# Performance work log

Measured on AMD Instinct MI355X. Metric: run time of the kernel, lower is better.

The kernel has to match this reference:

```python
import jax, jax.numpy as jnp
import numpy as np

EPS = 1e-5
H, D = 8, 64  # n_heads, head_n_channels


def _instance_norm(x):
    # x: [B, H, N, D]; InstanceNorm1d over grid axis N per (batch, head, channel)
    m = jnp.mean(x, axis=2, keepdims=True)
    v = jnp.var(x, axis=2, keepdims=True)
    return (x - m) * jax.lax.rsqrt(v + EPS)


def setup_inputs() -> dict:
    key = jax.random.key(0)
    ks = jax.random.split(key, 7)
    B, N, C, OUT = 4, 16384, 256, 256
    u_src = jax.random.normal(ks[0], (B, N, C), jnp.float32)
    pos_src = jax.random.uniform(ks[1], (B, N, 2), jnp.float32)
    s_in = 1.0 / np.sqrt(C)
    Wq = jax.random.normal(ks[2], (H * D, C), jnp.float32) * s_in
    Wk = jax.random.normal(ks[3], (H * D, C), jnp.float32) * s_in
    Wv = jax.random.normal(ks[4], (H * D, C), jnp.float32) * s_in
    Wo = jax.random.normal(ks[5], (OUT, H * D), jnp.float32) * (1.0 / np.sqrt(H * D))
    bo = jnp.zeros((OUT,), jnp.float32)
    return {"u_src": u_src, "pos_src": pos_src, "Wq": Wq, "Wk": Wk, "Wv": Wv, "Wo": Wo, "bo": bo}


def reference(u_src, pos_src, Wq, Wk, Wv, Wo, bo):
    B, N, C = u_src.shape
    # q/k/v projections -> [B, H, N, D]
    q = (u_src @ Wq.T).reshape(B, N, H, D).transpose(0, 2, 1, 3)
    k = (u_src @ Wk.T).reshape(B, N, H, D).transpose(0, 2, 1, 3)
    v = (u_src @ Wv.T).reshape(B, N, H, D).transpose(0, 2, 1, 3)
    # instance-norm k, v over the grid (domain) axis
    k = _instance_norm(k)
    v = _instance_norm(v)
    # associative linear attention with uniform quadrature weights 1/N
    w = 1.0 / N
    kv = jnp.einsum('bhnd,bhne->bhde', k, v * w)   # [B,H,D,D]
    u = jnp.einsum('bhnd,bhde->bhne', q, kv)       # [B,H,N,D]
    u = u.transpose(0, 2, 1, 3).reshape(B, N, H * D)
    return u @ Wo.T + bo
```

## Files before the change

kernel.cpp:

```cpp
#include <hip/hip_runtime.h>
#include <hip/hip_bf16.h>

#define BB    4
#define NTOT  16384
#define CC    256
#define HH    8
#define DD    64
#define HD    512
#define OUTC  256

typedef unsigned short u16;
typedef unsigned int u32;
typedef __attribute__((ext_vector_type(8))) short bf16x8;
typedef __attribute__((ext_vector_type(4))) float f32x4;
typedef __attribute__((ext_vector_type(4))) short u16x4;
typedef __attribute__((ext_vector_type(4))) u32 u32x4;

__device__ __forceinline__ float b2f(u16 u) {
    union { float f; u32 i; } x; x.i = ((u32)u) << 16; return x.f;
}
__device__ __forceinline__ u16 f2b(float f) {
    union { float f; u32 i; } x; x.f = f;
    u32 r = x.i + 0x7fffu + ((x.i >> 16) & 1u);
    return (u16)(r >> 16);
}

#define GLD(gp, lp) __builtin_amdgcn_global_load_lds( \
    (const __attribute__((address_space(1))) void*)(gp), \
    (__attribute__((address_space(3))) void*)(lp), 16, 0, 0)

#define MFMA(a, b, c) __builtin_amdgcn_mfma_f32_16x16x32_bf16((a), (b), (c), 0, 0, 0)

__global__ __launch_bounds__(256) void wcvt(
    const float* __restrict__ Wq, const float* __restrict__ Wk,
    const float* __restrict__ Wv, const float* __restrict__ Wo,
    u16* __restrict__ q, u16* __restrict__ k,
    u16* __restrict__ v, u16* __restrict__ o)
{
    const int z = blockIdx.z;
    const float* src = z == 0 ? Wq : z == 1 ? Wk : z == 2 ? Wv : Wo;
    u16* dst = z == 0 ? q : z == 1 ? k : z == 2 ? v : o;
    const int i = (blockIdx.x * 256 + threadIdx.x) * 8;
    const float4 a = *(const float4*)(src + i);
    const float4 b = *(const float4*)(src + i + 4);
    union { bf16x8 v; u16 s[8]; } w;
    w.s[0] = f2b(a.x); w.s[1] = f2b(a.y); w.s[2] = f2b(a.z); w.s[3] = f2b(a.w);
    w.s[4] = f2b(b.x); w.s[5] = f2b(b.y); w.s[6] = f2b(b.z); w.s[7] = f2b(b.w);
    *(bf16x8*)(dst + i) = w.v;
}

__global__ __launch_bounds__(512) void ggemm(
    const float* __restrict__ u, float* __restrict__ Gp, float* __restrict__ suP,
    u16* __restrict__ u_b)
{
    __shared__ u32 Ts[16 * 290];
    const int z = blockIdx.x, b = z >> 6, ck = z & 63;
    const float* base = u + (long long)b * NTOT * CC + (long long)ck * 256 * CC;
    u16* ub_base = u_b + (long long)b * NTOT * CC + (long long)ck * 256 * CC;
    const int t = threadIdx.x, w = t >> 6, l = t & 63;
    const int wy = w >> 1, wx = w & 1;
    const int r16 = l & 15, quad = l >> 4;
    const int sp = t >> 5;
    const int sq = t & 31;

    const int csa0 = 9 * ((wy * 64 + r16) >> 3) + (r16 & 7);
    const int csb0 = 9 * ((wx * 128 + r16) >> 3) + (r16 & 7);
    const int pr0 = 4 * quad * 290;

    f32x4 acc[4][8] = {};
    float su8[8] = {};

    float4 a0, a1, b0, b1;
    {
        const float* src = base + (long long)(2 * sp) * CC + sq * 8;
        a0 = *(const float4*)src;       a1 = *(const float4*)(src + 4);
        b0 = *(const float4*)(src + CC); b1 = *(const float4*)(src + CC + 4);
    }

    for (int it = 0; it < 8; it++) {
        {
            union { bf16x8 v; u16 q[8]; } ra, rb;
            ra.q[0] = f2b(a0.x); ra.q[1] = f2b(a0.y); ra.q[2] = f2b(a0.z); ra.q[3] = f2b(a0.w);
            ra.q[4] = f2b(a1.x); ra.q[5] = f2b(a1.y); ra.q[6] = f2b(a1.z); ra.q[7] = f2b(a1.w);
            rb.q[0] = f2b(b0.x); rb.q[1] = f2b(b0.y); rb.q[2] = f2b(b0.z); rb.q[3] = f2b(b0.w);
            rb.q[4] = f2b(b1.x); rb.q[5] = f2b(b1.y); rb.q[6] = f2b(b1.z); rb.q[7] = f2b(b1.w);
#pragma unroll
            for (int k = 0; k < 8; k++)
                su8[k] += b2f(ra.q[k]) + b2f(rb.q[k]);
            {
                u16* ub = ub_base + (long long)(it * 32 + 2 * sp) * CC + sq * 8;
                *(bf16x8*)ub = ra.v;
                *(bf16x8*)(ub + CC) = rb.v;
            }
            u32 pk[8];
#pragma unroll
            for (int k = 0; k < 8; k++)
                pk[k] = (u32)ra.q[k] | ((u32)rb.q[k] << 16);
            u32* dst = Ts + sp * 290 + 9 * sq;
#pragma unroll
            for (int k = 0; k < 8; k++) dst[k] = pk[k];
        }
        if (it < 7) {
            const float* src = base + (long long)((it + 1) * 32 + 2 * sp) * CC + sq * 8;
            a0 = *(const float4*)src;       a1 = *(const float4*)(src + 4);
            b0 = *(const float4*)(src + CC); b1 = *(const float4*)(src + CC + 4);
        }
        asm volatile("s_waitcnt lgkmcnt(0)" ::: "memory");
        __builtin_amdgcn_s_barrier();

        bf16x8 a[4], bb[8];
#pragma unroll
        for (int i = 0; i < 4; i++) {
            const int cs = csa0 + 18 * i;
            union { u32x4 u4; bf16x8 h; } f;
            f.u4[0] = Ts[pr0 + cs];       f.u4[1] = Ts[pr0 + 290 + cs];
            f.u4[2] = Ts[pr0 + 580 + cs]; f.u4[3] = Ts[pr0 + 870 + cs];
            a[i] = f.h;
        }
#pragma unroll
        for (int j = 0; j < 8; j++) {
            const int cs = csb0 + 18 * j;
            union { u32x4 u4; bf16x8 h; } f;
            f.u4[0] = Ts[pr0 + cs];       f.u4[1] = Ts[pr0 + 290 + cs];
            f.u4[2] = Ts[pr0 + 580 + cs]; f.u4[3] = Ts[pr0 + 870 + cs];
            bb[j] = f.h;
        }
#pragma unroll
        for (int i = 0; i < 4; i++)
#pragma unroll
            for (int j = 0; j < 8; j++)
                acc[i][j] = MFMA(a[i], bb[j], acc[i][j]);
        asm volatile("" ::: "memory");
        __builtin_amdgcn_s_barrier();
    }

    float* Cp = Gp + (long long)z * 65536;
#pragma unroll
    for (int i = 0; i < 4; i++)
#pragma unroll
        for (int j = 0; j < 8; j++)
#pragma unroll
            for (int rr = 0; rr < 4; rr++)
                Cp[(wy * 64 + 16 * i + quad * 4 + rr) * 256 + wx * 128 + 16 * j + r16]
                    = acc[i][j][rr];

    float* S = (float*)Ts;
#pragma unroll
    for (int k = 0; k < 8; k++) S[sp * 264 + sq * 8 + k] = su8[k];
    __syncthreads();
    if (t < 256) {
        float s = 0.f;
#pragma unroll
        for (int p = 0; p < 16; p++) s += S[p * 264 + t];
        suP[z * 256 + t] = s;
    }
}

__global__ __launch_bounds__(256) void gred(
    const float* __restrict__ Gp, const float* __restrict__ suP,
    u16* __restrict__ Gb, float* __restrict__ su)
{
    const int b = blockIdx.y, t = threadIdx.x;
    const int row = blockIdx.x * 4 + (t >> 6);
    const int col = (t & 63) * 4;
    const float* p = Gp + (long long)(b * 64) * 65536 + row * 256 + col;
    f32x4 s = {};
#pragma unroll
    for (int ck = 0; ck < 64; ck++) {
        f32x4 v = *(const f32x4*)(p + (long long)ck * 65536);
        s[0] += v[0]; s[1] += v[1]; s[2] += v[2]; s[3] += v[3];
    }
    union { u16x4 v; u16 q[4]; } pk;
#pragma unroll
    for (int k = 0; k < 4; k++) pk.q[k] = f2b(s[k]);
    *(u16x4*)(Gb + (long long)b * 65536 + row * 256 + col) = pk.v;

    if (blockIdx.x == 0) {
        float s2 = 0.f;
#pragma unroll
        for (int ck = 0; ck < 64; ck++) s2 += suP[(b * 64 + ck) * 256 + t];
        su[b * 256 + t] = s2;
    }
}

__global__ __launch_bounds__(256) void skvz(
    const u16* __restrict__ P2, const float* __restrict__ su,
    const u16* __restrict__ Wk_b, const u16* __restrict__ Wv_b,
    const u16* __restrict__ Wq_b, u16* __restrict__ Zt)
{
    __shared__ u16 pool[20480];
    __shared__ float mkL[64], rkL[64], mvL[64], rvL[64];

    const int bx = blockIdx.x, b = bx >> 3, h = bx & 7;
    const int t = threadIdx.x, w = t >> 6, l = t & 63;
    const int r16 = l & 15, quad = l >> 4;

    const u16* WkH = Wk_b + (h * 64) * 256;
    const u16* WvH = Wv_b + (h * 64) * 256;
    const u16* PkH = P2 + (long long)b * 262144 + (h * 64) * 256;
    const u16* PvH = P2 + (long long)b * 262144 + (512 + h * 64) * 256;

    {
        const int row = t >> 1, half = t & 1;
        const u16* Prow = (row < 64 ? PkH + row * 256 : PvH + (row - 64) * 256) + half * 128;
        const u16* Wrow = (row < 64 ? WkH + row * 256 : WvH + (row - 64) * 256) + half * 128;
        const float* suB = su + b * 256 + half * 128;
        float e2 = 0.f, m = 0.f;
#pragma unroll
        for (int c8 = 0; c8 < 16; c8++) {
            bf16x8 pw = *(const bf16x8*)(Prow + c8 * 8);
            bf16x8 ww = *(const bf16x8*)(Wrow + c8 * 8);
#pragma unroll
            for (int k = 0; k < 8; k++) {
                const float wv_ = b2f((u16)ww[k]);
                e2 += b2f((u16)pw[k]) * wv_;
                m  += wv_ * suB[c8 * 8 + k];
            }
        }
        e2 += __shfl_xor(e2, 1);
        m  += __shfl_xor(m, 1);
        if (half == 0) {
            m *= (1.0f / NTOT);
            const float r = rsqrtf(e2 * (1.0f / NTOT) - m * m + 1e-5f);
            if (row < 64) { mkL[row] = m; rkL[row] = r; }
            else          { mvL[row - 64] = m; rvL[row - 64] = r; }
        }
    }
    __syncthreads();

    const int mh = (w >> 1) * 32, nh = (w & 1) * 32;
    float mkR[2][4], rkR[2][4], mvR[2], rvR[2];
#pragma unroll
    for (int i = 0; i < 2; i++)
#pragma unroll
        for (int rr = 0; rr < 4; rr++) {
            mkR[i][rr] = mkL[mh + 16 * i + quad * 4 + rr];
            rkR[i][rr] = rkL[mh + 16 * i + quad * 4 + rr];
        }
#pragma unroll
    for (int j = 0; j < 2; j++) {
        mvR[j] = mvL[nh + 16 * j + r16];
        rvR[j] = rvL[nh + 16 * j + r16];
    }

    f32x4 accs[2][2] = {};
    for (int ch = 0; ch < 8; ch++) {
        const int ko = quad * 8;
        bf16x8 ap[2], bv[2];
#pragma unroll
        for (int i = 0; i < 2; i++)
            ap[i] = *(const bf16x8*)(PkH + (mh + 16 * i + r16) * 256 + ch * 32 + ko);
#pragma unroll
        for (int j = 0; j < 2; j++)
            bv[j] = *(const bf16x8*)(WvH + (nh + 16 * j + r16) * 256 + ch * 32 + ko);
#pragma unroll
        for (int i = 0; i < 2; i++)
#pragma unroll
            for (int j = 0; j < 2; j++)
                accs[i][j] = MFMA(ap[i], bv[j], accs[i][j]);
    }

    u16* kvTL = pool;
    u16* WqTL = pool + 4096;
#pragma unroll
    for (int i = 0; i < 2; i++)
#pragma unroll
        for (int j = 0; j < 2; j++)
#pragma unroll
            for (int rr = 0; rr < 4; rr++) {
                const int d = mh + 16 * i + quad * 4 + rr;
                const int e = nh + 16 * j + r16;
                const float kv = rkR[i][rr] * rvR[j] *
                    (accs[i][j][rr] * (1.0f / NTOT) - mkR[i][rr] * mvR[j]);
                kvTL[(d >> 5) * 2048 + e * 32 + (d & 31)] = f2b(kv);
            }
    {
        const int d = t >> 2, q = t & 3;
        const u16* Wrow = Wq_b + (h * 64 + d) * 256 + q * 64;
#pragma unroll
        for (int s = 0; s < 8; s++) {
            bf16x8 raw = *(const bf16x8*)(Wrow + s * 8);
#pragma unroll
            for (int k = 0; k < 8; k++) {
                const int c = q * 64 + s * 8 + k;
                WqTL[(d >> 5) * 8192 + c * 32 + (d & 31)] = (u16)raw[k];
            }
        }
    }
    __syncthreads();

    f32x4 accy[4][4] = {};
#pragma unroll
    for (int ch = 0; ch < 2; ch++) {
        const int ko = quad * 8;
        bf16x8 akv[4], bq[4];
#pragma unroll
        for (int i = 0; i < 4; i++)
            akv[i] = *(const bf16x8*)(kvTL + ch * 2048 + (16 * i + r16) * 32 + ko);
#pragma unroll
        for (int j = 0; j < 4; j++)
            bq[j] = *(const bf16x8*)(WqTL + ch * 8192 + (w * 64 + 16 * j + r16) * 32 + ko);
#pragma unroll
        for (int i = 0; i < 4; i++)
#pragma unroll
            for (int j = 0; j < 4; j++)
                accy[i][j] = MFMA(akv[i], bq[j], accy[i][j]);
    }
#pragma unroll
    for (int i = 0; i < 4; i++)
#pragma unroll
        for (int j = 0; j < 4; j++) {
            const int c = w * 64 + 16 * j + r16;
            const int e0 = 16 * i + quad * 4;
            union { u16x4 v; u16 s[4]; } pk;
#pragma unroll
            for (int rr = 0; rr < 4; rr++) pk.s[rr] = f2b(accy[i][j][rr]);
            *(u16x4*)(Zt + ((long long)(b * 256 + c)) * 512 + h * 64 + e0) = pk.v;
        }
}

template <typename CT>
__global__ __launch_bounds__(256) void gemm_bt(
    const u16* __restrict__ A, const u16* __restrict__ Bm,
    CT* __restrict__ C, const float* __restrict__ bias,
    int K, int lda, int ldc,
    long long aStride, long long bStride, long long cStride)
{
    __shared__ u16 As[128 * 32];
    __shared__ u16 Bs[128 * 32];

    const int bz = blockIdx.z;
    A  += (long long)bz * aStride;
    Bm += (long long)bz * bStride;
    C  += (long long)bz * cStride;

    const int m0 = blockIdx.x * 128;
    const int n0 = blockIdx.y * 128;
    const int t  = threadIdx.x;
    const int wv = t >> 6, l = t & 63;
    const int wy = wv >> 1, wx = wv & 1;
    const int r16  = l & 15;
    const int quad = l >> 4;
    const int srow = wv * 16 + (l >> 2);
    const int scol = (l & 3) * 8;

    f32x4 acc[4][4] = {};

    for (int kk = 0; kk < K; kk += 32) {
#pragma unroll
        for (int s = 0; s < 2; s++) {
            GLD(A + (long long)(m0 + s * 64 + srow) * lda + kk + scol,
                As + s * 2048 + wv * 512);
            GLD(Bm + (long long)(n0 + s * 64 + srow) * K + kk + scol,
                Bs + s * 2048 + wv * 512);
        }
        __syncthreads();

        bf16x8 a[4], b[4];
#pragma unroll
        for (int i = 0; i < 4; i++)
            a[i] = *(const bf16x8*)(As + (wy * 64 + 16 * i + r16) * 32 + quad * 8);
#pragma unroll
        for (int j = 0; j < 4; j++)
            b[j] = *(const bf16x8*)(Bs + (wx * 64 + 16 * j + r16) * 32 + quad * 8);
#pragma unroll
        for (int i = 0; i < 4; i++)
#pragma unroll
            for (int j = 0; j < 4; j++)
                acc[i][j] = MFMA(a[i], b[j], acc[i][j]);
        __syncthreads();
    }

#pragma unroll
    for (int j = 0; j < 4; j++) {
        const int col = n0 + wx * 64 + 16 * j + r16;
        const float bv = bias ? bias[col] : 0.0f;
#pragma unroll
        for (int i = 0; i < 4; i++) {
#pragma unroll
            for (int r = 0; r < 4; r++) {
                const int row = m0 + wy * 64 + 16 * i + quad * 4 + r;
                const float v = acc[i][j][r] + bv;
                if constexpr (sizeof(CT) == 2) C[(long long)row * ldc + col] = f2b(v);
                else                           C[(long long)row * ldc + col] = v;
            }
        }
    }
}

__global__ __launch_bounds__(1024) void gemm_out(
    const u16* __restrict__ Au, const u16* __restrict__ Ft,
    float* __restrict__ C, const float* __restrict__ bias)
{
    __shared__ u16 As[128 * 32];
    __shared__ u16 Bs[256 * 32];

    const int b = blockIdx.z;
    Au += (long long)b * NTOT * CC;
    const u16* Bm = Ft + (long long)b * 65536;
    C += (long long)b * NTOT * OUTC;

    const int m0 = blockIdx.x * 128;
    const int t  = threadIdx.x;
    const int wv = t >> 6, l = t & 63;
    const int wy = wv >> 2, wx = wv & 3;
    const int r16  = l & 15;
    const int quad = l >> 4;
    const int srow = t >> 2;
    const int scol = (t & 3) * 8;

    f32x4 acc[2][4] = {};

    for (int kk = 0; kk < 256; kk += 32) {
        GLD(Bm + (long long)srow * 256 + kk + scol, Bs + srow * 32 + scol);
        if (t < 512)
            GLD(Au + (long long)(m0 + srow) * CC + kk + scol, As + srow * 32 + scol);
        __syncthreads();

        bf16x8 a[2], bb[4];
#pragma unroll
        for (int i = 0; i < 2; i++)
            a[i] = *(const bf16x8*)(As + (wy * 32 + 16 * i + r16) * 32 + quad * 8);
#pragma unroll
        for (int j = 0; j < 4; j++)
            bb[j] = *(const bf16x8*)(Bs + (wx * 64 + 16 * j + r16) * 32 + quad * 8);
#pragma unroll
        for (int i = 0; i < 2; i++)
#pragma unroll
            for (int j = 0; j < 4; j++)
                acc[i][j] = MFMA(a[i], bb[j], acc[i][j]);
        __syncthreads();
    }

#pragma unroll
    for (int j = 0; j < 4; j++) {
        const int col = wx * 64 + 16 * j + r16;
        const float bv = bias[col];
#pragma unroll
        for (int i = 0; i < 2; i++) {
#pragma unroll
            for (int r = 0; r < 4; r++) {
                const int row = m0 + wy * 32 + 16 * i + quad * 4 + r;
                C[(long long)row * OUTC + col] = acc[i][j][r] + bv;
            }
        }
    }
}

extern "C" void kernel_launch(void* const* d_in, const int* in_sizes, int n_in,
                              void* d_out, int out_size, void* d_ws, size_t ws_size,
                              hipStream_t stream)
{
    const float* u_src = (const float*)d_in[0];
    const float* Wq = (const float*)d_in[2];
    const float* Wk = (const float*)d_in[3];
    const float* Wv = (const float*)d_in[4];
    const float* Wo = (const float*)d_in[5];
    const float* bo = (const float*)d_in[6];
    float* out = (float*)d_out;

    char* ws = (char*)d_ws;
    size_t off = 0;
    float* Gp  = (float*)(ws + off); off += 67108864;
    float* suP = (float*)(ws + off); off += 262144;
    u16*  Gb   = (u16*)(ws + off);  off += 524288;
    u16*  Wq_b = (u16*)(ws + off);  off += 262144;
    u16*  Wk_b = (u16*)(ws + off);  off += 262144;
    u16*  Wv_b = (u16*)(ws + off);  off += 262144;
    u16*  Wo_b = (u16*)(ws + off);  off += 262144;
    float* su  = (float*)(ws + off); off += 4096;
    u16*  Zt   = (u16*)(ws + off);  off += 1048576;
    u16*  Ft   = (u16*)(ws + off);  off += 524288;
    u16*  P2   = (u16*)(ws + off);  off += 2097152;
    u16*  u_b  = (u16*)(ws + off);  off += 33554432;

    const dim3 blk(256);

    wcvt<<<dim3(64, 1, 4), blk, 0, stream>>>(Wq, Wk, Wv, Wo, Wq_b, Wk_b, Wv_b, Wo_b);

    ggemm<<<dim3(BB * 64), dim3(512), 0, stream>>>(u_src, Gp, suP, u_b);
    gred<<<dim3(64, BB), blk, 0, stream>>>(Gp, suP, Gb, su);

    gemm_bt<u16><<<dim3(8, 2, BB), blk, 0, stream>>>(
        Wk_b, Gb, P2, nullptr, 256, 256, 256, 0, 65536, 262144);

    skvz<<<dim3(BB * HH), blk, 0, stream>>>(P2, su, Wk_b, Wv_b, Wq_b, Zt);

    gemm_bt<u16><<<dim3(2, 2, BB), blk, 0, stream>>>(
        Wo_b, Zt, Ft, nullptr, 512, 512, 256, 0, 131072, 65536);

    gemm_out<<<dim3(128, 1, BB), dim3(1024), 0, stream>>>(u_b, Ft, out, bo);
}
```

Baseline: 210.4 us.

## Split Gram GEMM output rows across block pairs with longer K-chunks

The u^T u Gram kernel now gives each block a 512-row chunk of the grid axis and half of the 256x256 output, pairing two blocks per chunk that are spaced 8 apart in launch order so they likely share u reads through cache. Each block loads twice as many rows per iteration and accumulates a 128x256 tile with 8 waves each holding 64x64. Only the half==0 block writes the bf16 copy of u and the column sums. The partial-sum buffer halves from 64 to 32 chunks per batch, which cuts the fp32 partial-G traffic written by ggemm and read by the reduction kernel. In exchange each fp32 row of u is read from global memory twice, once per half.

```diff
diff --git a/kernel.cpp b/kernel.cpp
--- a/kernel.cpp
+++ b/kernel.cpp
@@ -53,106 +53,125 @@
     const float* __restrict__ u, float* __restrict__ Gp, float* __restrict__ suP,
     u16* __restrict__ u_b)
 {
-    __shared__ u32 Ts[16 * 290];
-    const int z = blockIdx.x, b = z >> 6, ck = z & 63;
-    const float* base = u + (long long)b * NTOT * CC + (long long)ck * 256 * CC;
-    u16* ub_base = u_b + (long long)b * NTOT * CC + (long long)ck * 256 * CC;
+    __shared__ u32 Ts[32 * 290];
+    const int z = blockIdx.x;
+    const int half = (z >> 3) & 1;
+    const int cg = ((z >> 4) << 3) | (z & 7);
+    const int b = cg >> 5, ck = cg & 31;
+    const float* base = u + (long long)b * NTOT * CC + (long long)ck * 512 * CC;
+    u16* ub_base = u_b + (long long)b * NTOT * CC + (long long)ck * 512 * CC;
     const int t = threadIdx.x, w = t >> 6, l = t & 63;
-    const int wy = w >> 1, wx = w & 1;
+    const int wy = w >> 2, wx = w & 3;
     const int r16 = l & 15, quad = l >> 4;
     const int sp = t >> 5;
     const int sq = t & 31;
 
-    const int csa0 = 9 * ((wy * 64 + r16) >> 3) + (r16 & 7);
-    const int csb0 = 9 * ((wx * 128 + r16) >> 3) + (r16 & 7);
-    const int pr0 = 4 * quad * 290;
-
-    f32x4 acc[4][8] = {};
+    const int csa0 = 9 * ((half * 128 + wy * 64 + r16) >> 3) + (r16 & 7);
+    const int csb0 = 9 * ((wx * 64 + r16) >> 3) + (r16 & 7);
+
+    f32x4 acc[4][4] = {};
     float su8[8] = {};
 
-    float4 a0, a1, b0, b1;
+    float4 a0, a1, b0, b1, c0, c1, d0, d1;
     {
-        const float* src = base + (long long)(2 * sp) * CC + sq * 8;
-        a0 = *(const float4*)src;       a1 = *(const float4*)(src + 4);
-        b0 = *(const float4*)(src + CC); b1 = *(const float4*)(src + CC + 4);
+        const float* s1 = base + (long long)(2 * sp) * CC + sq * 8;
+        const float* s2 = s1 + 32 * CC;
+        a0 = *(const float4*)s1;        a1 = *(const float4*)(s1 + 4);
+        b0 = *(const float4*)(s1 + CC); b1 = *(const float4*)(s1 + CC + 4);
+        c0 = *(const float4*)s2;        c1 = *(const float4*)(s2 + 4);
+        d0 = *(const float4*)(s2 + CC); d1 = *(const float4*)(s2 + CC + 4);
     }
 
     for (int it = 0; it < 8; it++) {
+        __syncthreads();
         {
-            union { bf16x8 v; u16 q[8]; } ra, rb;
+            union { bf16x8 v; u16 q[8]; } ra, rb, rc, rd;
             ra.q[0] = f2b(a0.x); ra.q[1] = f2b(a0.y); ra.q[2] = f2b(a0.z); ra.q[3] = f2b(a0.w);
             ra.q[4] = f2b(a1.x); ra.q[5] = f2b(a1.y); ra.q[6] = f2b(a1.z); ra.q[7] = f2b(a1.w);
             rb.q[0] = f2b(b0.x); rb.q[1] = f2b(b0.y); rb.q[2] = f2b(b0.z); rb.q[3] = f2b(b0.w);
             rb.q[4] = f2b(b1.x); rb.q[5] = f2b(b1.y); rb.q[6] = f2b(b1.z); rb.q[7] = f2b(b1.w);
-#pragma unroll
-            for (int k = 0; k < 8; k++)
-                su8[k] += b2f(ra.q[k]) + b2f(rb.q[k]);
-            {
-                u16* ub = ub_base + (long long)(it * 32 + 2 * sp) * CC + sq * 8;
+            rc.q[0] = f2b(c0.x); rc.q[1] = f2b(c0.y); rc.q[2] = f2b(c0.z); rc.q[3] = f2b(c0.w);
+            rc.q[4] = f2b(c1.x); rc.q[5] = f2b(c1.y); rc.q[6] = f2b(c1.z); rc.q[7] = f2b(c1.w);
+            rd.q[0] = f2b(d0.x); rd.q[1] = f2b(d0.y); rd.q[2] = f2b(d0.z); rd.q[3] = f2b(d0.w);
+            rd.q[4] = f2b(d1.x); rd.q[5] = f2b(d1.y); rd.q[6] = f2b(d1.z); rd.q[7] = f2b(d1.w);
+            if (half == 0) {
+#pragma unroll
+                for (int k = 0; k < 8; k++)
+                    su8[k] += (b2f(ra.q[k]) + b2f(rb.q[k])) + (b2f(rc.q[k]) + b2f(rd.q[k]));
+                u16* ub = ub_base + (long long)(it * 64 + 2 * sp) * CC + sq * 8;
                 *(bf16x8*)ub = ra.v;
                 *(bf16x8*)(ub + CC) = rb.v;
-            }
-            u32 pk[8];
-#pragma unroll
-            for (int k = 0; k < 8; k++)
-                pk[k] = (u32)ra.q[k] | ((u32)rb.q[k] << 16);
-            u32* dst = Ts + sp * 290 + 9 * sq;
-#pragma unroll
-            for (int k = 0; k < 8; k++) dst[k] = pk[k];
+                *(bf16x8*)(ub + 32 * CC) = rc.v;
+                *(bf16x8*)(ub + 33 * CC) = rd.v;
+            }
+            u32* dst1 = Ts + sp * 290 + 9 * sq;
+            u32* dst2 = Ts + (sp + 16) * 290 + 9 * sq;
+#pragma unroll
+            for (int k = 0; k < 8; k++) {
+                dst1[k] = (u32)ra.q[k] | ((u32)rb.q[k] << 16);
+                dst2[k] = (u32)rc.q[k] | ((u32)rd.q[k] << 16);
+            }
         }
         if (it < 7) {
-            const float* src = base + (long long)((it + 1) * 32 + 2 * sp) * CC + sq * 8;
-            a0 = *(const float4*)src;       a1 = *(const float4*)(src + 4);
-            b0 = *(const float4*)(src + CC); b1 = *(const float4*)(src + CC + 4);
-        }
-        asm volatile("s_waitcnt lgkmcnt(0)" ::: "memory");
-        __builtin_amdgcn_s_barrier();
-
-        bf16x8 a[4], bb[8];
-#pragma unroll
-        for (int i = 0; i < 4; i++) {
-            const int cs = csa0 + 18 * i;
-            union { u32x4 u4; bf16x8 h; } f;
-            f.u4[0] = Ts[pr0 + cs];       f.u4[1] = Ts[pr0 + 290 + cs];
-            f.u4[2] = Ts[pr0 + 580 + cs]; f.u4[3] = Ts[pr0 + 870 + cs];
-            a[i] = f.h;
-        }
-#pragma unroll
-        for (int j = 0; j < 8; j++) {
-            const int cs = csb0 + 18 * j;
-            union { u32x4 u4; bf16x8 h; } f;
-            f.u4[0] = Ts[pr0 + cs];       f.u4[1] = Ts[pr0 + 290 + cs];
-            f.u4[2] = Ts[pr0 + 580 + cs]; f.u4[3] = Ts[pr0 + 870 + cs];
-            bb[j] = f.h;
-        }
-#pragma unroll
-        for (int i = 0; i < 4; i++)
-#pragma unroll
-            for (int j = 0; j < 8; j++)
-                acc[i][j] = MFMA(a[i], bb[j], acc[i][j]);
-        asm volatile("" ::: "memory");
-        __builtin_amdgcn_s_barrier();
-    }
-
-    float* Cp = Gp + (long long)z * 65536;
+            const float* s1 = base + (long long)((it + 1) * 64 + 2 * sp) * CC + sq * 8;
+            const float* s2 = s1 + 32 * CC;
+            a0 = *(const float4*)s1;        a1 = *(const float4*)(s1 + 4);
+            b0 = *(const float4*)(s1 + CC); b1 = *(const float4*)(s1 + CC + 4);
+            c0 = *(const float4*)s2;        c1 = *(const float4*)(s2 + 4);
+            d0 = *(const float4*)(s2 + CC); d1 = *(const float4*)(s2 + CC + 4);
+        }
+        __syncthreads();
+
+#pragma unroll
+        for (int kb = 0; kb < 2; kb++) {
+            const int pr0 = (kb * 16 + 4 * quad) * 290;
+            bf16x8 a[4], bb[4];
+#pragma unroll
+            for (int i = 0; i < 4; i++) {
+                const int cs = pr0 + csa0 + 18 * i;
+                union { u32x4 u4; bf16x8 h; } f;
+                f.u4[0] = Ts[cs];       f.u4[1] = Ts[290 + cs];
+                f.u4[2] = Ts[580 + cs]; f.u4[3] = Ts[870 + cs];
+                a[i] = f.h;
+            }
+#pragma unroll
+            for (int j = 0; j < 4; j++) {
+                const int cs = pr0 + csb0 + 18 * j;
+                union { u32x4 u4; bf16x8 h; } f;
+                f.u4[0] = Ts[cs];       f.u4[1] = Ts[290 + cs];
+                f.u4[2] = Ts[580 + cs]; f.u4[3] = Ts[870 + cs];
+                bb[j] = f.h;
+            }
+#pragma unroll
+            for (int i = 0; i < 4; i++)
+#pragma unroll
+                for (int j = 0; j < 4; j++)
+                    acc[i][j] = MFMA(a[i], bb[j], acc[i][j]);
+        }
+    }
+
+    float* Cp = Gp + (long long)cg * 65536;
 #pragma unroll
     for (int i = 0; i < 4; i++)
 #pragma unroll
-        for (int j = 0; j < 8; j++)
+        for (int j = 0; j < 4; j++)
 #pragma unroll
             for (int rr = 0; rr < 4; rr++)
-                Cp[(wy * 64 + 16 * i + quad * 4 + rr) * 256 + wx * 128 + 16 * j + r16]
-                    = acc[i][j][rr];
-
-    float* S = (float*)Ts;
-#pragma unroll
-    for (int k = 0; k < 8; k++) S[sp * 264 + sq * 8 + k] = su8[k];
-    __syncthreads();
-    if (t < 256) {
-        float s = 0.f;
-#pragma unroll
-        for (int p = 0; p < 16; p++) s += S[p * 264 + t];
-        suP[z * 256 + t] = s;
+                Cp[(half * 128 + wy * 64 + 16 * i + quad * 4 + rr) * 256
+                   + wx * 64 + 16 * j + r16] = acc[i][j][rr];
+
+    if (half == 0) {
+        __syncthreads();
+        float* S = (float*)Ts;
+#pragma unroll
+        for (int k = 0; k < 8; k++) S[sp * 264 + sq * 8 + k] = su8[k];
+        __syncthreads();
+        if (t < 256) {
+            float s = 0.f;
+#pragma unroll
+            for (int p = 0; p < 16; p++) s += S[p * 264 + t];
+            suP[cg * 256 + t] = s;
+        }
     }
 }
 
@@ -163,10 +182,10 @@
     const int b = blockIdx.y, t = threadIdx.x;
     const int row = blockIdx.x * 4 + (t >> 6);
     const int col = (t & 63) * 4;
-    const float* p = Gp + (long long)(b * 64) * 65536 + row * 256 + col;
+    const float* p = Gp + (long long)(b * 32) * 65536 + row * 256 + col;
     f32x4 s = {};
 #pragma unroll
-    for (int ck = 0; ck < 64; ck++) {
+    for (int ck = 0; ck < 32; ck++) {
         f32x4 v = *(const f32x4*)(p + (long long)ck * 65536);
         s[0] += v[0]; s[1] += v[1]; s[2] += v[2]; s[3] += v[3];
     }
@@ -178,7 +197,7 @@
     if (blockIdx.x == 0) {
         float s2 = 0.f;
 #pragma unroll
-        for (int ck = 0; ck < 64; ck++) s2 += suP[(b * 64 + ck) * 256 + t];
+        for (int ck = 0; ck < 32; ck++) s2 += suP[(b * 32 + ck) * 256 + t];
         su[b * 256 + t] = s2;
     }
 }
@@ -461,8 +480,8 @@
 
     char* ws = (char*)d_ws;
     size_t off = 0;
-    float* Gp  = (float*)(ws + off); off += 67108864;
-    float* suP = (float*)(ws + off); off += 262144;
+    float* Gp  = (float*)(ws + off); off += 33554432;
+    float* suP = (float*)(ws + off); off += 131072;
     u16*  Gb   = (u16*)(ws + off);  off += 524288;
     u16*  Wq_b = (u16*)(ws + off);  off += 262144;
     u16*  Wk_b = (u16*)(ws + off);  off += 262144;
@@ -478,7 +497,7 @@
 
     wcvt<<<dim3(64, 1, 4), blk, 0, stream>>>(Wq, Wk, Wv, Wo, Wq_b, Wk_b, Wv_b, Wo_b);
 
-    ggemm<<<dim3(BB * 64), dim3(512), 0, stream>>>(u_src, Gp, suP, u_b);
+    ggemm<<<dim3(256), dim3(512), 0, stream>>>(u_src, Gp, suP, u_b);
     gred<<<dim3(64, BB), blk, 0, stream>>>(Gp, suP, Gb, su);
 
     gemm_bt<u16><<<dim3(8, 2, BB), blk, 0, stream>>>(
```

Result: faster. 204.6 us (-2.8%).
